# Optimization experiments

Measured on AMD Instinct MI355X. Metric: run time of the kernel, lower is better.

Reference implementation:

```python
import jax, jax.numpy as jnp
import numpy as np

ACCEL_LIMIT = 1.0
OMEGA_LIMIT = 1.0
B, N_IN, H1, H21, H22 = 32768, 8, 2048, 1024, 1024
N_CL = 2


def setup_inputs() -> dict:
    key = jax.random.key(0)
    ks = jax.random.split(key, 16)
    def g(k, shape, scale):
        return (jax.random.normal(k, shape, dtype=jnp.float32) * scale)
    inp = {
        "x": jax.random.normal(ks[0], (B, N_IN), dtype=jnp.float32),
        "W1": g(ks[1], (N_IN, H1), (2.0 / N_IN) ** 0.5),
        "b1": jnp.zeros((H1,), jnp.float32),
        "W21": g(ks[2], (H1, H21), (2.0 / H1) ** 0.5),
        "b21": jnp.zeros((H21,), jnp.float32),
        "W31": g(ks[3], (H21, N_CL), (1.0 / H21) ** 0.5),
        "b31": jnp.zeros((N_CL,), jnp.float32),
        "W22": g(ks[4], (H1, H22), (2.0 / H1) ** 0.5),
        "b22": jnp.zeros((H22,), jnp.float32),
        "W32": g(ks[5], (H22, N_CL), (1.0 / H22) ** 0.5),
        "b32": jnp.zeros((N_CL,), jnp.float32),
        "input_mean": jax.random.normal(ks[6], (N_IN,), dtype=jnp.float32),
        "input_std": jax.random.uniform(ks[7], (N_IN,), jnp.float32, 0.5, 1.5),
        "output_mean": jax.random.normal(ks[8], (N_CL,), dtype=jnp.float32) * 0.1,
        "output_std": jax.random.uniform(ks[9], (N_CL,), jnp.float32, 0.5, 1.5),
        "s0": jnp.ones((1,), jnp.float32),
        "s1": jnp.ones((1,), jnp.float32),
        "s2": jnp.ones((1,), jnp.float32),
        "s3": jnp.ones((1,), jnp.float32),
        "sgn": 1,
    }
    return inp


def reference(x, W1, b1, W21, b21, W31, b31, W22, b22, W32, b32,
              input_mean, input_std, output_mean, output_std,
              s0, s1, s2, s3, sgn):
    # De-normalized raw state (used by disabled liveness branch; kept for fidelity)
    x0 = x * input_std + input_mean  # [B, N_IN]
    h = jax.nn.relu(x @ W1 + b1)                 # [B, H1]
    x31 = jax.nn.relu(h @ W21 + b21) @ W31 + b31  # reference control, [B, 2]
    x32 = 4.0 * jax.nn.sigmoid(jax.nn.relu(h @ W22 + b22) @ W32 + b32)  # HOCBF penalties (unused in limits-only QP)
    x31_actual = x31 * output_std + output_mean   # [B, 2]

    # QP: min 0.5 u^T I u + x31_actual^T u  s.t. box constraints from control limits.
    # G rows: [0,1]<=a+s0, [0,-1]<=a+s1, [1,0]<=w+s2, [-1,0]<=w+s3.
    # Q=I and axis-aligned constraints -> closed form: u = clip(-p, lower, upper).
    upper = jnp.concatenate([OMEGA_LIMIT + s2, ACCEL_LIMIT + s0])   # [2]
    lower = jnp.concatenate([-(OMEGA_LIMIT + s3), -(ACCEL_LIMIT + s1)])  # [2]
    u = jnp.minimum(jnp.maximum(-x31_actual, lower), upper)         # [B, 2]

    out = (u - output_mean) / output_std
    return out
```

## Files before the change

### kernel.cpp

```cpp
#include <hip/hip_runtime.h>
#include <hip/hip_bf16.h>
#include <hip/hip_fp16.h>

#define DEVI __device__ __forceinline__

typedef _Float16 f16x8 __attribute__((ext_vector_type(8)));
typedef float f32x4 __attribute__((ext_vector_type(4)));

static constexpr int M = 32768;
static constexpr int N = 1024;
static constexpr int K = 2048;
static constexpr int BM = 256, BN = 256, BK = 32;
static constexpr int NT = K / BK;
static constexpr int NSTRIP = (N / BN) * 4;

static constexpr size_t WS_H    = 0;
static constexpr size_t WS_W21T = 134217728;
static constexpr size_t WS_PART = 134217728 + 4194304;

using lds_vp = __attribute__((address_space(3))) void*;
using gbl_vp = const __attribute__((address_space(1))) void*;

DEVI void async_ld16(const void* g, void* l) {
  __builtin_amdgcn_global_load_lds((gbl_vp)(size_t)g,
                                   (lds_vp)(uint32_t)(size_t)l,
                                   16, 0, 0);
}

__global__ __launch_bounds__(256)
void w21cvt_kernel(const float* __restrict__ W21, _Float16* __restrict__ w21t) {
  __shared__ float sT[64][65];
  const int tid = threadIdx.x;
  const int k0 = blockIdx.x * 64;
  const int n0 = blockIdx.y * 64;
  const int row = tid >> 2;
#pragma unroll
  for (int q = 0; q < 4; ++q) {
    int c = (tid & 3) * 4 + q * 16;
    float4 v = *(const float4*)(W21 + (size_t)(k0 + row) * 1024 + n0 + c);
    sT[row][c + 0] = v.x; sT[row][c + 1] = v.y;
    sT[row][c + 2] = v.z; sT[row][c + 3] = v.w;
  }
  __syncthreads();
  const int n  = tid >> 2;
  const int kc = (tid & 3) * 16;
  union { _Float16 h[16]; float4 f4[2]; } u;
#pragma unroll
  for (int e = 0; e < 16; ++e) u.h[e] = (_Float16)sT[kc + e][n];
  float4* dst = (float4*)(w21t + (size_t)(n0 + n) * 2048 + k0 + kc);
  dst[0] = u.f4[0]; dst[1] = u.f4[1];
}

__global__ __launch_bounds__(256)
void gemm1_kernel(const float* __restrict__ x, const float* __restrict__ W1,
                  const float* __restrict__ b1, _Float16* __restrict__ hout) {
  __shared__ float sx[64 * 8];
  const int tid = threadIdx.x;
  const int r0 = blockIdx.x * 64;
  if (tid < 128) {
    *(float4*)&sx[tid * 4] = *(const float4*)(x + (size_t)r0 * 8 + tid * 4);
  }
  float w1r[8][8];
#pragma unroll
  for (int j = 0; j < 8; ++j) {
    *(float4*)&w1r[j][0] = *(const float4*)(W1 + j * 2048 + tid * 8);
    *(float4*)&w1r[j][4] = *(const float4*)(W1 + j * 2048 + tid * 8 + 4);
  }
  float bb[8];
  *(float4*)&bb[0] = *(const float4*)(b1 + tid * 8);
  *(float4*)&bb[4] = *(const float4*)(b1 + tid * 8 + 4);
  __syncthreads();
  for (int r = 0; r < 64; ++r) {
    float xv[8];
    *(float4*)&xv[0] = *(float4*)&sx[r * 8];
    *(float4*)&xv[4] = *(float4*)&sx[r * 8 + 4];
    float acc[8];
#pragma unroll
    for (int c = 0; c < 8; ++c) acc[c] = bb[c];
#pragma unroll
    for (int j = 0; j < 8; ++j)
#pragma unroll
      for (int c = 0; c < 8; ++c) acc[c] = fmaf(xv[j], w1r[j][c], acc[c]);
    union { f16x8 v; float4 f4; } u;
#pragma unroll
    for (int c = 0; c < 8; ++c) u.v[c] = (_Float16)fmaxf(acc[c], 0.f);
    *(float4*)(hout + (size_t)(r0 + r) * 2048 + tid * 8) = u.f4;
  }
}

__global__ __launch_bounds__(512, 2)
void gemm2_kernel(const _Float16* __restrict__ h, const _Float16* __restrict__ w21t,
                  const float* __restrict__ b21, const float* __restrict__ w31,
                  float* __restrict__ part) {
  __shared__ __align__(16) _Float16 sA[4 * BM * BK];
  __shared__ __align__(16) _Float16 sB[4 * BN * BK];

  const int tid  = threadIdx.x;
  const int lane = tid & 63;
  const int w    = tid >> 6;
  const int wr   = w >> 2;
  const int wc   = w & 3;

  const int lin  = blockIdx.x;
  const int swz  = (lin & 7) * 64 + (lin >> 3);
  const int nblk = swz & 3;
  const int mblk = swz >> 2;
  const int r0 = mblk * BM;
  const int n0 = nblk * BN;

  f32x4 acc[8][4] = {};

  const int sr  = tid >> 2;
  const int scp = tid & 3;
  const int sc  = scp ^ ((sr >> 2) & 3);
  const _Float16* gAb = h    + (size_t)(r0 + sr) * K + sc * 8;
  const _Float16* gBb = w21t + (size_t)(n0 + sr) * K + sc * 8;
  char* const lA0 = (char*)&sA[0] + tid * 16;
  char* const lB0 = (char*)&sB[0] + tid * 16;

  auto stageA = [&](int tt) {
    const int b = tt & 3;
    const _Float16* g = gAb + tt * BK;
    async_ld16(g,                    lA0 + b * 16384);
    async_ld16(g + (size_t)128 * K,  lA0 + b * 16384 + 8192);
  };
  auto stageB = [&](int tt) {
    const int b = tt & 3;
    const _Float16* g = gBb + tt * BK;
    async_ld16(g,                    lB0 + b * 16384);
    async_ld16(g + (size_t)128 * K,  lB0 + b * 16384 + 8192);
  };

  const int arow  = wr * 128 + (lane & 15);
  const int brow  = wc * 64  + (lane & 15);
  const int klo   = lane >> 4;
  const int abyte = arow * 64 + ((klo ^ ((arow >> 2) & 3)) * 16);
  const int bbyte = brow * 64 + ((klo ^ ((brow >> 2) & 3)) * 16);

  stageA(0); stageB(0);
  stageA(1); stageB(1);
  stageA(2); stageB(2);
  asm volatile("s_waitcnt vmcnt(8)" ::: "memory");
  __builtin_amdgcn_s_barrier();

  for (int t = 0; t < NT; ++t) {
    const int buf = t & 3;
    const char* pA = (const char*)&sA[0] + buf * 16384;
    const char* pB = (const char*)&sB[0] + buf * 16384;

    f16x8 aF[8], bF[4];
#pragma unroll
    for (int m = 0; m < 8; ++m) aF[m] = *(const f16x8*)(pA + abyte + m * 1024);
    bF[0] = *(const f16x8*)(pB + bbyte);
    bF[1] = *(const f16x8*)(pB + bbyte + 1024);
    if (t + 3 < NT) stageA(t + 3);
    __builtin_amdgcn_s_barrier();
    asm volatile("s_waitcnt lgkmcnt(0)" ::: "memory");
    __builtin_amdgcn_sched_barrier(0);
    __builtin_amdgcn_s_setprio(1);
#pragma unroll
    for (int m = 0; m < 8; ++m) {
      acc[m][0] = __builtin_amdgcn_mfma_f32_16x16x32_f16(aF[m], bF[0], acc[m][0], 0, 0, 0);
      acc[m][1] = __builtin_amdgcn_mfma_f32_16x16x32_f16(aF[m], bF[1], acc[m][1], 0, 0, 0);
    }
    __builtin_amdgcn_s_setprio(0);
    __builtin_amdgcn_sched_barrier(0);
    __builtin_amdgcn_s_barrier();

    bF[2] = *(const f16x8*)(pB + bbyte + 2048);
    bF[3] = *(const f16x8*)(pB + bbyte + 3072);
    if (t + 3 < NT) stageB(t + 3);
    if (t < NT - 3)       asm volatile("s_waitcnt vmcnt(8)" ::: "memory");
    else if (t == NT - 3) asm volatile("s_waitcnt vmcnt(4)" ::: "memory");
    else                  asm volatile("s_waitcnt vmcnt(0)" ::: "memory");
    __builtin_amdgcn_s_barrier();
    asm volatile("s_waitcnt lgkmcnt(0)" ::: "memory");
    __builtin_amdgcn_sched_barrier(0);
    __builtin_amdgcn_s_setprio(1);
#pragma unroll
    for (int m = 0; m < 8; ++m) {
      acc[m][2] = __builtin_amdgcn_mfma_f32_16x16x32_f16(aF[m], bF[2], acc[m][2], 0, 0, 0);
      acc[m][3] = __builtin_amdgcn_mfma_f32_16x16x32_f16(aF[m], bF[3], acc[m][3], 0, 0, 0);
    }
    __builtin_amdgcn_s_setprio(0);
    __builtin_amdgcn_sched_barrier(0);
    __builtin_amdgcn_s_barrier();
  }

  float bb[4], w0v[4], w1v[4];
#pragma unroll
  for (int n = 0; n < 4; ++n) {
    int cg = n0 + wc * 64 + n * 16 + (lane & 15);
    bb[n]  = b21[cg];
    w0v[n] = w31[cg * 2 + 0];
    w1v[n] = w31[cg * 2 + 1];
  }
  const int strip = nblk * 4 + wc;
#pragma unroll
  for (int m = 0; m < 8; ++m) {
#pragma unroll
    for (int j = 0; j < 4; ++j) {
      float s0 = 0.f, s1 = 0.f;
#pragma unroll
      for (int n = 0; n < 4; ++n) {
        float a = fmaxf(acc[m][n][j] + bb[n], 0.f);
        s0 = fmaf(a, w0v[n], s0);
        s1 = fmaf(a, w1v[n], s1);
      }
#pragma unroll
      for (int d = 1; d < 16; d <<= 1) {
        s0 += __shfl_xor(s0, d, 64);
        s1 += __shfl_xor(s1, d, 64);
      }
      if ((lane & 15) == 0) {
        int gr = r0 + wr * 128 + m * 16 + (lane >> 4) * 4 + j;
        float2 v; v.x = s0; v.y = s1;
        *(float2*)(part + ((size_t)strip * M + gr) * 2) = v;
      }
    }
  }
}

__global__ __launch_bounds__(256)
void final_kernel(const float* __restrict__ part, const float* __restrict__ b31,
                  const float* __restrict__ om, const float* __restrict__ os,
                  const float* __restrict__ s0p, const float* __restrict__ s1p,
                  const float* __restrict__ s2p, const float* __restrict__ s3p,
                  float* __restrict__ out) {
  const int r = blockIdx.x * blockDim.x + threadIdx.x;
  float a0 = b31[0], a1 = b31[1];
#pragma unroll
  for (int s = 0; s < NSTRIP; ++s) {
    float2 v = *(const float2*)(part + ((size_t)s * M + r) * 2);
    a0 += v.x; a1 += v.y;
  }
  const float om0 = om[0], om1 = om[1], os0 = os[0], os1 = os[1];
  const float xa0 = a0 * os0 + om0;
  const float xa1 = a1 * os1 + om1;
  const float up0 = 1.0f + s2p[0];
  const float up1 = 1.0f + s0p[0];
  const float lo0 = -(1.0f + s3p[0]);
  const float lo1 = -(1.0f + s1p[0]);
  const float u0 = fminf(fmaxf(-xa0, lo0), up0);
  const float u1 = fminf(fmaxf(-xa1, lo1), up1);
  float2 o; o.x = (u0 - om0) / os0; o.y = (u1 - om1) / os1;
  *(float2*)(out + (size_t)r * 2) = o;
}

extern "C" void kernel_launch(void* const* d_in, const int* in_sizes, int n_in,
                              void* d_out, int out_size, void* d_ws, size_t ws_size,
                              hipStream_t stream) {
  const float* x    = (const float*)d_in[0];
  const float* W1   = (const float*)d_in[1];
  const float* b1   = (const float*)d_in[2];
  const float* W21  = (const float*)d_in[3];
  const float* b21  = (const float*)d_in[4];
  const float* W31  = (const float*)d_in[5];
  const float* b31  = (const float*)d_in[6];
  const float* omean = (const float*)d_in[13];
  const float* ostd  = (const float*)d_in[14];
  const float* s0 = (const float*)d_in[15];
  const float* s1 = (const float*)d_in[16];
  const float* s2 = (const float*)d_in[17];
  const float* s3 = (const float*)d_in[18];
  float* out = (float*)d_out;

  char* ws = (char*)d_ws;
  _Float16* hbuf = (_Float16*)(ws + WS_H);
  _Float16* w21t = (_Float16*)(ws + WS_W21T);
  float*    part = (float*)(ws + WS_PART);

  w21cvt_kernel<<<dim3(32, 16), dim3(256), 0, stream>>>(W21, w21t);
  gemm1_kernel<<<dim3(512), dim3(256), 0, stream>>>(x, W1, b1, hbuf);
  gemm2_kernel<<<dim3((M / BM) * (N / BN)), dim3(512), 0, stream>>>(hbuf, w21t, b21, W31, part);
  final_kernel<<<dim3(M / 256), dim3(256), 0, stream>>>(part, b31, omean, ostd,
                                                        s0, s1, s2, s3, out);
}
```

Measured before the change: 172.5 us.

## Use BK=64 double-buffered pipeline with half-stage prefetch and LDS epilogue reduction

Doubles the K tile to 64 in the fp16 MFMA GEMM and replaces the 4-deep BK=32 ring with a 2-deep buffer of 64-wide K tiles, each loaded in two 32-wide halves. Prefetches are spread across four compute phases per iteration, which halves the loop trip count and per-tile barrier overhead. The LDS swizzle changes to an additive rotation scheme. The epilogue replaces the 16-lane shuffle reduction with an LDS scratch write followed by a cooperative float4 sum. The cost is 128 KB of LDS per block, which may limit blocks per CU below the launch-bounds target of 2.

```diff
diff --git a/kernel.cpp b/kernel.cpp
--- a/kernel.cpp
+++ b/kernel.cpp
@@ -10,7 +10,7 @@
 static constexpr int M = 32768;
 static constexpr int N = 1024;
 static constexpr int K = 2048;
-static constexpr int BM = 256, BN = 256, BK = 32;
+static constexpr int BM = 256, BN = 256, BK = 64;
 static constexpr int NT = K / BK;
 static constexpr int NSTRIP = (N / BN) * 4;
 
@@ -92,8 +92,7 @@
 void gemm2_kernel(const _Float16* __restrict__ h, const _Float16* __restrict__ w21t,
                   const float* __restrict__ b21, const float* __restrict__ w31,
                   float* __restrict__ part) {
-  __shared__ __align__(16) _Float16 sA[4 * BM * BK];
-  __shared__ __align__(16) _Float16 sB[4 * BN * BK];
+  __shared__ __align__(16) char smem[131072];
 
   const int tid  = threadIdx.x;
   const int lane = tid & 63;
@@ -110,78 +109,108 @@
 
   f32x4 acc[8][4] = {};
 
-  const int sr  = tid >> 2;
-  const int scp = tid & 3;
-  const int sc  = scp ^ ((sr >> 2) & 3);
-  const _Float16* gAb = h    + (size_t)(r0 + sr) * K + sc * 8;
-  const _Float16* gBb = w21t + (size_t)(n0 + sr) * K + sc * 8;
-  char* const lA0 = (char*)&sA[0] + tid * 16;
-  char* const lB0 = (char*)&sB[0] + tid * 16;
-
-  auto stageA = [&](int tt) {
-    const int b = tt & 3;
-    const _Float16* g = gAb + tt * BK;
-    async_ld16(g,                    lA0 + b * 16384);
-    async_ld16(g + (size_t)128 * K,  lA0 + b * 16384 + 8192);
+  const int cA = ((tid & 3) - (tid >> 3)) & 3;
+  const _Float16* pA = h    + (size_t)(r0 + (tid >> 2)) * K + cA * 8;
+  const _Float16* pB = w21t + (size_t)(n0 + (tid >> 2)) * K + cA * 8;
+  char* const lbase = smem + tid * 16;
+
+  auto stageA = [&](int t, int hs) {
+    const _Float16* g = pA + t * 64 + hs * 32;
+    char* l = lbase + (t & 1) * 65536 + hs * 16384;
+    async_ld16(g,                     l);
+    async_ld16(g + (size_t)128 * K,   l + 8192);
   };
-  auto stageB = [&](int tt) {
-    const int b = tt & 3;
-    const _Float16* g = gBb + tt * BK;
-    async_ld16(g,                    lB0 + b * 16384);
-    async_ld16(g + (size_t)128 * K,  lB0 + b * 16384 + 8192);
+  auto stageB = [&](int t, int hs) {
+    const _Float16* g = pB + t * 64 + hs * 32;
+    char* l = lbase + (t & 1) * 65536 + 32768 + hs * 16384;
+    async_ld16(g,                     l);
+    async_ld16(g + (size_t)128 * K,   l + 8192);
   };
 
-  const int arow  = wr * 128 + (lane & 15);
-  const int brow  = wc * 64  + (lane & 15);
-  const int klo   = lane >> 4;
-  const int abyte = arow * 64 + ((klo ^ ((arow >> 2) & 3)) * 16);
-  const int bbyte = brow * 64 + ((klo ^ ((brow >> 2) & 3)) * 16);
-
-  stageA(0); stageB(0);
-  stageA(1); stageB(1);
-  stageA(2); stageB(2);
-  asm volatile("s_waitcnt vmcnt(8)" ::: "memory");
+  const int arow0 = wr * 128 + (lane & 15);
+  const int aslot = ((lane >> 4) + (arow0 >> 1)) & 3;
+  const int abyte = arow0 * 64 + aslot * 16;
+  const int brow0 = wc * 64 + (lane & 15);
+  const int bslot = ((lane >> 4) + (brow0 >> 1)) & 3;
+  const int bbyte = 32768 + brow0 * 64 + bslot * 16;
+
+  stageB(0, 0); stageA(0, 0); stageB(0, 1); stageA(0, 1);
+  stageB(1, 0); stageA(1, 0); stageB(1, 1);
+  asm volatile("s_waitcnt vmcnt(10)" ::: "memory");
   __builtin_amdgcn_s_barrier();
 
   for (int t = 0; t < NT; ++t) {
-    const int buf = t & 3;
-    const char* pA = (const char*)&sA[0] + buf * 16384;
-    const char* pB = (const char*)&sB[0] + buf * 16384;
-
-    f16x8 aF[8], bF[4];
-#pragma unroll
-    for (int m = 0; m < 8; ++m) aF[m] = *(const f16x8*)(pA + abyte + m * 1024);
-    bF[0] = *(const f16x8*)(pB + bbyte);
-    bF[1] = *(const f16x8*)(pB + bbyte + 1024);
-    if (t + 3 < NT) stageA(t + 3);
+    const char* base = smem + (t & 1) * 65536;
+    f16x8 aF[4], bF[4];
+
+#pragma unroll
+    for (int m = 0; m < 4; ++m) aF[m] = *(const f16x8*)(base + abyte + m * 1024);
+#pragma unroll
+    for (int n = 0; n < 4; ++n) bF[n] = *(const f16x8*)(base + bbyte + n * 1024);
+    if (t + 1 < NT) stageA(t + 1, 1);
     __builtin_amdgcn_s_barrier();
     asm volatile("s_waitcnt lgkmcnt(0)" ::: "memory");
     __builtin_amdgcn_sched_barrier(0);
     __builtin_amdgcn_s_setprio(1);
 #pragma unroll
-    for (int m = 0; m < 8; ++m) {
-      acc[m][0] = __builtin_amdgcn_mfma_f32_16x16x32_f16(aF[m], bF[0], acc[m][0], 0, 0, 0);
-      acc[m][1] = __builtin_amdgcn_mfma_f32_16x16x32_f16(aF[m], bF[1], acc[m][1], 0, 0, 0);
-    }
+    for (int m = 0; m < 4; ++m)
+#pragma unroll
+      for (int n = 0; n < 4; ++n)
+        acc[m][n] = __builtin_amdgcn_mfma_f32_16x16x32_f16(aF[m], bF[n], acc[m][n], 0, 0, 0);
     __builtin_amdgcn_s_setprio(0);
     __builtin_amdgcn_sched_barrier(0);
     __builtin_amdgcn_s_barrier();
 
-    bF[2] = *(const f16x8*)(pB + bbyte + 2048);
-    bF[3] = *(const f16x8*)(pB + bbyte + 3072);
-    if (t + 3 < NT) stageB(t + 3);
-    if (t < NT - 3)       asm volatile("s_waitcnt vmcnt(8)" ::: "memory");
-    else if (t == NT - 3) asm volatile("s_waitcnt vmcnt(4)" ::: "memory");
-    else                  asm volatile("s_waitcnt vmcnt(0)" ::: "memory");
+#pragma unroll
+    for (int m = 0; m < 4; ++m) aF[m] = *(const f16x8*)(base + abyte + (m + 4) * 1024);
+    if (t + 2 < NT) stageB(t + 2, 0);
+    if (t < NT - 2) asm volatile("s_waitcnt vmcnt(10)" ::: "memory");
+    else            asm volatile("s_waitcnt vmcnt(0)"  ::: "memory");
     __builtin_amdgcn_s_barrier();
     asm volatile("s_waitcnt lgkmcnt(0)" ::: "memory");
     __builtin_amdgcn_sched_barrier(0);
     __builtin_amdgcn_s_setprio(1);
 #pragma unroll
-    for (int m = 0; m < 8; ++m) {
-      acc[m][2] = __builtin_amdgcn_mfma_f32_16x16x32_f16(aF[m], bF[2], acc[m][2], 0, 0, 0);
-      acc[m][3] = __builtin_amdgcn_mfma_f32_16x16x32_f16(aF[m], bF[3], acc[m][3], 0, 0, 0);
-    }
+    for (int m = 0; m < 4; ++m)
+#pragma unroll
+      for (int n = 0; n < 4; ++n)
+        acc[m + 4][n] = __builtin_amdgcn_mfma_f32_16x16x32_f16(aF[m], bF[n], acc[m + 4][n], 0, 0, 0);
+    __builtin_amdgcn_s_setprio(0);
+    __builtin_amdgcn_sched_barrier(0);
+    __builtin_amdgcn_s_barrier();
+
+#pragma unroll
+    for (int m = 0; m < 4; ++m) aF[m] = *(const f16x8*)(base + 16384 + abyte + m * 1024);
+#pragma unroll
+    for (int n = 0; n < 4; ++n) bF[n] = *(const f16x8*)(base + 16384 + bbyte + n * 1024);
+    if (t + 2 < NT) stageA(t + 2, 0);
+    __builtin_amdgcn_s_barrier();
+    asm volatile("s_waitcnt lgkmcnt(0)" ::: "memory");
+    __builtin_amdgcn_sched_barrier(0);
+    __builtin_amdgcn_s_setprio(1);
+#pragma unroll
+    for (int m = 0; m < 4; ++m)
+#pragma unroll
+      for (int n = 0; n < 4; ++n)
+        acc[m][n] = __builtin_amdgcn_mfma_f32_16x16x32_f16(aF[m], bF[n], acc[m][n], 0, 0, 0);
+    __builtin_amdgcn_s_setprio(0);
+    __builtin_amdgcn_sched_barrier(0);
+    __builtin_amdgcn_s_barrier();
+
+#pragma unroll
+    for (int m = 0; m < 4; ++m) aF[m] = *(const f16x8*)(base + 16384 + abyte + (m + 4) * 1024);
+    if (t + 2 < NT) stageB(t + 2, 1);
+    if (t < NT - 2) asm volatile("s_waitcnt vmcnt(10)" ::: "memory");
+    else            asm volatile("s_waitcnt vmcnt(0)"  ::: "memory");
+    __builtin_amdgcn_s_barrier();
+    asm volatile("s_waitcnt lgkmcnt(0)" ::: "memory");
+    __builtin_amdgcn_sched_barrier(0);
+    __builtin_amdgcn_s_setprio(1);
+#pragma unroll
+    for (int m = 0; m < 4; ++m)
+#pragma unroll
+      for (int n = 0; n < 4; ++n)
+        acc[m + 4][n] = __builtin_amdgcn_mfma_f32_16x16x32_f16(aF[m], bF[n], acc[m + 4][n], 0, 0, 0);
     __builtin_amdgcn_s_setprio(0);
     __builtin_amdgcn_sched_barrier(0);
     __builtin_amdgcn_s_barrier();
@@ -195,7 +224,7 @@
     w0v[n] = w31[cg * 2 + 0];
     w1v[n] = w31[cg * 2 + 1];
   }
-  const int strip = nblk * 4 + wc;
+  float* red = (float*)smem;
 #pragma unroll
   for (int m = 0; m < 8; ++m) {
 #pragma unroll
@@ -207,17 +236,29 @@
         s0 = fmaf(a, w0v[n], s0);
         s1 = fmaf(a, w1v[n], s1);
       }
-#pragma unroll
-      for (int d = 1; d < 16; d <<= 1) {
-        s0 += __shfl_xor(s0, d, 64);
-        s1 += __shfl_xor(s1, d, 64);
-      }
-      if ((lane & 15) == 0) {
-        int gr = r0 + wr * 128 + m * 16 + (lane >> 4) * 4 + j;
-        float2 v; v.x = s0; v.y = s1;
-        *(float2*)(part + ((size_t)strip * M + gr) * 2) = v;
-      }
+      int row_local = m * 16 + (lane >> 4) * 4 + j;
+      int idx = w * 4096 + row_local * 32 + (lane & 15) * 2;
+      red[idx]     = s0;
+      red[idx + 1] = s1;
     }
+  }
+  __syncthreads();
+#pragma unroll
+  for (int q = tid; q < 1024; q += 512) {
+    const int w2 = q >> 7, rl = q & 127;
+    const float* src = red + w2 * 4096 + rl * 32;
+    float a0 = 0.f, a1 = 0.f;
+#pragma unroll
+    for (int k = 0; k < 8; ++k) {
+      int kk = (k + (tid & 7)) & 7;
+      float4 v = *(const float4*)(src + kk * 4);
+      a0 += v.x + v.z;
+      a1 += v.y + v.w;
+    }
+    int gr = r0 + (w2 >> 2) * 128 + rl;
+    int strip = nblk * 4 + (w2 & 3);
+    float2 o; o.x = a0; o.y = a1;
+    *(float2*)(part + ((size_t)strip * M + gr) * 2) = o;
   }
 }
 
```

Measured after the change: 152.3 us. -11.7%, faster.
